# Performance work log

Measured on AMD Instinct MI355X. Metric: run time of the kernel, lower is better.

## Reference

```python
import jax, jax.numpy as jnp
import numpy as np

N_NODES = 50000
N_EDGES = 800000
IN_DIM = 128
HID = 64
HEADS = 4
SLOPE = 0.01


def edge_softmax(e, dst, n):
    # e: [E, H] logits, softmax over edges sharing the same destination node
    m = jax.ops.segment_max(e, dst, num_segments=n)          # [N, H]
    ex = jnp.exp(e - m[dst])                                 # [E, H]
    s = jax.ops.segment_sum(ex, dst, num_segments=n)         # [N, H]
    return ex / s[dst]


def gat_conv(h, src, dst, W, attn_l, attn_r, bias, n, heads, out_dim):
    ft = (h @ W).reshape(n, heads, out_dim)                  # [N, H, D]
    el = jnp.sum(ft * attn_l, axis=-1)                       # [N, H]
    er = jnp.sum(ft * attn_r, axis=-1)                       # [N, H]
    e = jax.nn.leaky_relu(el[src] + er[dst], SLOPE)          # [E, H]
    a = edge_softmax(e, dst, n)                              # [E, H]
    msg = ft[src] * a[:, :, None]                            # [E, H, D]
    out = jax.ops.segment_sum(msg, dst, num_segments=n)      # [N, H, D]
    return out + bias.reshape(1, heads, out_dim)


def setup_inputs() -> dict:
    key = jax.random.key(0)
    ks = jax.random.split(key, 12)
    inputs = jax.random.normal(ks[0], (N_NODES, IN_DIM), dtype=jnp.float32)
    src = jax.random.randint(ks[1], (N_EDGES,), 0, N_NODES, dtype=jnp.int32)
    dst = jax.random.randint(ks[2], (N_EDGES,), 0, N_NODES, dtype=jnp.int32)
    s1 = 1.0 / np.sqrt(IN_DIM)
    W1 = jax.random.normal(ks[3], (IN_DIM, HEADS * HID), dtype=jnp.float32) * s1
    al1 = jax.random.normal(ks[4], (HEADS, HID), dtype=jnp.float32) * 0.1
    ar1 = jax.random.normal(ks[5], (HEADS, HID), dtype=jnp.float32) * 0.1
    b1 = jnp.zeros((HEADS * HID,), dtype=jnp.float32)
    s2 = 1.0 / np.sqrt(HEADS * HID)
    W2 = jax.random.normal(ks[6], (HEADS * HID, HID), dtype=jnp.float32) * s2
    al2 = jax.random.normal(ks[7], (1, HID), dtype=jnp.float32) * 0.1
    ar2 = jax.random.normal(ks[8], (1, HID), dtype=jnp.float32) * 0.1
    b2 = jnp.zeros((HID,), dtype=jnp.float32)
    return {"inputs": inputs, "src": src, "dst": dst,
            "W1": W1, "al1": al1, "ar1": ar1, "b1": b1,
            "W2": W2, "al2": al2, "ar2": ar2, "b2": b2}


def reference(inputs, src, dst, W1, al1, ar1, b1, W2, al2, ar2, b2):
    # layer 1: multi-head, activation elu, flatten heads
    h = gat_conv(inputs, src, dst, W1, al1, ar1, b1, N_NODES, HEADS, HID)
    h = jax.nn.elu(h).reshape(N_NODES, HEADS * HID)
    # layer 2 (last): single head
    h = gat_conv(h, src, dst, W2, al2, ar2, b2, N_NODES, 1, HID)
    h = jax.nn.elu(h).reshape(N_NODES, HID)
    return h
```

## Files before the change

kernel.cpp:

```cpp
#include <hip/hip_runtime.h>
#include <hip/hip_bf16.h>
#include <math.h>

#define N_NODES 50000
#define N_EDGES 800000
#define IN_DIM 128
#define HID 64
#define HEADS 4

typedef unsigned short ushort_t;
typedef __attribute__((ext_vector_type(8))) short bf16x8;
typedef __attribute__((ext_vector_type(4))) float f32x4;

static __device__ __forceinline__ ushort_t f2bf(float f) {
  __hip_bfloat16 b = __float2bfloat16(f);
  return *(ushort_t*)&b;
}
static __device__ __forceinline__ float bflo(unsigned d) {
  union { unsigned u; float f; } c; c.u = d << 16; return c.f;
}
static __device__ __forceinline__ float bfhi(unsigned d) {
  union { unsigned u; float f; } c; c.u = d & 0xffff0000u; return c.f;
}
static __device__ __forceinline__ unsigned packbf(float lo, float hi) {
  return (unsigned)f2bf(lo) | ((unsigned)f2bf(hi) << 16);
}
static __device__ __forceinline__ float lrelu(float x) {
  return (x > 0.f) ? x : 0.01f * x;
}

__global__ __launch_bounds__(256) void k_cvt_hist(const float* __restrict__ w1,
                                                  const float* __restrict__ w2,
                                                  ushort_t* __restrict__ bpk1,
                                                  ushort_t* __restrict__ bpk2,
                                                  const int* __restrict__ dst,
                                                  int* __restrict__ cnt,
                                                  int* __restrict__ slot) {
  constexpr int NP1 = 4096;
  constexpr int NP2 = 2048;
  constexpr int CVT_BLK = (NP1 + NP2) / 256;
  int bid = blockIdx.x;
  if (bid < CVT_BLK) {
    int t = bid * 256 + threadIdx.x;
    if (t < NP1) {
      int l = t & 63, rem = t >> 6;
      int kk = rem & 3, ct = (rem >> 2) & 3, hh = rem >> 4;
      int kb = kk * 32 + (l >> 4) * 8;
      int col = hh * 64 + ct * 16 + (l & 15);
      ushort_t v[8];
      #pragma unroll
      for (int j = 0; j < 8; ++j) v[j] = f2bf(w1[(kb + j) * 256 + col]);
      *(uint4*)&bpk1[t * 8] = *(uint4*)v;
    } else {
      int u = t - NP1;
      int l = u & 63, rem = u >> 6;
      int kk = rem & 7, ct = rem >> 3;
      int kb = kk * 32 + (l >> 4) * 8;
      int col = ct * 16 + (l & 15);
      ushort_t v[8];
      #pragma unroll
      for (int j = 0; j < 8; ++j) v[j] = f2bf(w2[(kb + j) * 64 + col]);
      *(uint4*)&bpk2[u * 8] = *(uint4*)v;
    }
  } else {
    int e = (bid - CVT_BLK) * 256 + threadIdx.x;
    if (e < N_EDGES) {
      int d = dst[e];
      int p = atomicAdd(&cnt[d], 1);
      slot[e] = p;
    }
  }
}

__global__ __launch_bounds__(512) void k_scan_gemm1(const int* __restrict__ cnt,
                                                    int* __restrict__ offp,
                                                    int* __restrict__ bsum,
                                                    const float* __restrict__ A,
                                                    const ushort_t* __restrict__ Bpk,
                                                    ushort_t* __restrict__ C,
                                                    const float* __restrict__ al,
                                                    const float* __restrict__ ar,
                                                    float* __restrict__ el,
                                                    float* __restrict__ er, int M) {
  __shared__ char smraw[128 * 40 * 2];
  const int tid = threadIdx.x;
  if (blockIdx.x < 49) {
    int* lds = (int*)smraw;
    int i = blockIdx.x * 1024 + tid * 2;
    int v0 = (i < N_NODES) ? cnt[i] : 0;
    int v1 = (i + 1 < N_NODES) ? cnt[i + 1] : 0;
    int t = v0 + v1;
    lds[tid] = t;
    __syncthreads();
    for (int s = 1; s < 512; s <<= 1) {
      int u = (tid >= s) ? lds[tid - s] : 0;
      __syncthreads();
      lds[tid] += u;
      __syncthreads();
    }
    int excl = lds[tid] - t;
    if (i < N_NODES) offp[i] = excl;
    if (i + 1 < N_NODES) offp[i + 1] = excl + v0;
    if (tid == 511) bsum[blockIdx.x] = lds[511];
    return;
  }
  ushort_t (*As)[40] = (ushort_t(*)[40])smraw;
  const int m0 = (blockIdx.x - 49) * 128;
  const int w = tid >> 6, l = tid & 63;
  const int hh = w >> 1, rh = (w & 1) * 64;
  const int lr = l & 15, lk = l >> 4;
  f32x4 acc[4][4] = {};

  #pragma unroll
  for (int kk = 0; kk < 4; ++kk) {
    int k0 = kk * 32;
    {
      int r = tid >> 2, kc = (tid & 3) * 8;
      float4 va = make_float4(0.f, 0.f, 0.f, 0.f), vb = va;
      if (m0 + r < M) {
        va = *(const float4*)&A[(size_t)(m0 + r) * IN_DIM + k0 + kc];
        vb = *(const float4*)&A[(size_t)(m0 + r) * IN_DIM + k0 + kc + 4];
      }
      uint4 p;
      p.x = packbf(va.x, va.y); p.y = packbf(va.z, va.w);
      p.z = packbf(vb.x, vb.y); p.w = packbf(vb.z, vb.w);
      *(uint4*)&As[r][kc] = p;
    }
    __syncthreads();
    bf16x8 a[4];
    #pragma unroll
    for (int rt = 0; rt < 4; ++rt) a[rt] = *(const bf16x8*)&As[rh + rt * 16 + lr][lk * 8];
    #pragma unroll
    for (int ct = 0; ct < 4; ++ct) {
      bf16x8 b = ((const bf16x8*)Bpk)[((hh * 4 + ct) * 4 + kk) * 64 + l];
      #pragma unroll
      for (int rt = 0; rt < 4; ++rt)
        acc[rt][ct] = __builtin_amdgcn_mfma_f32_16x16x32_bf16(a[rt], b, acc[rt][ct], 0, 0, 0);
    }
    __syncthreads();
  }
  float ala[4], ara[4];
  #pragma unroll
  for (int ct = 0; ct < 4; ++ct) {
    ala[ct] = al[hh * 64 + ct * 16 + lr];
    ara[ct] = ar[hh * 64 + ct * 16 + lr];
  }
  #pragma unroll
  for (int rt = 0; rt < 4; ++rt)
    #pragma unroll
    for (int j = 0; j < 4; ++j) {
      float pel = 0.f, per = 0.f;
      #pragma unroll
      for (int ct = 0; ct < 4; ++ct) {
        float v = acc[rt][ct][j];
        pel = fmaf(v, ala[ct], pel);
        per = fmaf(v, ara[ct], per);
      }
      #pragma unroll
      for (int o = 1; o <= 8; o <<= 1) {
        pel += __shfl_xor(pel, o);
        per += __shfl_xor(per, o);
      }
      int row = m0 + rh + rt * 16 + lk * 4 + j;
      if (lr == 0 && row < M) { el[row * 4 + hh] = pel; er[row * 4 + hh] = per; }
    }
  #pragma unroll
  for (int rt = 0; rt < 4; ++rt)
    #pragma unroll
    for (int ct = 0; ct < 4; ++ct)
      #pragma unroll
      for (int j = 0; j < 4; ++j) {
        int row = m0 + rh + rt * 16 + lk * 4 + j;
        if (row < M) C[(size_t)row * 256 + hh * 64 + ct * 16 + lr] = f2bf(acc[rt][ct][j]);
      }
}

__global__ __launch_bounds__(256) void k_place(const int* __restrict__ offp,
                                               const int* __restrict__ bsum,
                                               int* __restrict__ off,
                                               const int* __restrict__ src,
                                               const int* __restrict__ dst,
                                               const int* __restrict__ slot,
                                               int* __restrict__ ssrc) {
  __shared__ int pref[64];
  const int tid = threadIdx.x;
  const int bid = blockIdx.x;
  if (bid < 49) {
    if (tid < 64) {
      int v = (tid < bid) ? bsum[tid] : 0;
      #pragma unroll
      for (int o = 1; o < 64; o <<= 1) v += __shfl_xor(v, o);
      if (tid == 0) pref[0] = v;
    }
    __syncthreads();
    int e0 = pref[0];
    int i = bid * 1024 + tid * 4;
    if (i + 3 < N_NODES) {
      int4 q = *(const int4*)&offp[i];
      *(int4*)&off[i] = make_int4(q.x + e0, q.y + e0, q.z + e0, q.w + e0);
    } else {
      if (i < N_NODES) off[i] = offp[i] + e0;
      if (i + 1 < N_NODES) off[i + 1] = offp[i + 1] + e0;
      if (i + 2 < N_NODES) off[i + 2] = offp[i + 2] + e0;
      if (i + 3 < N_NODES) off[i + 3] = offp[i + 3] + e0;
    }
    if (bid == 0 && tid == 0) off[N_NODES] = N_EDGES;
    return;
  }
  if (tid < 64) {
    int v = (tid < 49) ? bsum[tid] : 0;
    int orig = v;
    #pragma unroll
    for (int o = 1; o < 64; o <<= 1) { int u = __shfl_up(v, o); if (tid >= o) v += u; }
    pref[tid] = v - orig;
  }
  __syncthreads();
  int e = (bid - 49) * 256 + tid;
  if (e < N_EDGES) {
    int d = dst[e];
    ssrc[offp[d] + pref[d >> 10] + slot[e]] = src[e];
  }
}

__global__ __launch_bounds__(256) void agg4f_k(const ushort_t* __restrict__ ftb,
                                               const float* __restrict__ el,
                                               const float* __restrict__ er,
                                               const int* __restrict__ off,
                                               const int* __restrict__ ssrc,
                                               const float* __restrict__ bias,
                                               ushort_t* __restrict__ outb) {
  __shared__ float wl[4][64][4];
  __shared__ int srcl[4][64];
  int wv = threadIdx.x >> 6, lane = threadIdx.x & 63;
  int n = blockIdx.x * 4 + wv;
  if (n >= N_NODES) return;
  int s0 = off[n], s1 = off[n + 1];
  int half = lane >> 5, sl = lane & 31;
  int head = sl >> 3;
  const float4* el4 = (const float4*)el;
  float4 erv = ((const float4*)er)[n];
  float4 sum = make_float4(0.f, 0.f, 0.f, 0.f);
  float acc[8] = {};
  for (int c = s0; c < s1; c += 64) {
    int e = c + lane;
    float4 ex = make_float4(0.f, 0.f, 0.f, 0.f);
    int s = 0;
    if (e < s1) {
      s = ssrc[e];
      float4 q = el4[s];
      ex.x = __expf(lrelu(q.x + erv.x));
      ex.y = __expf(lrelu(q.y + erv.y));
      ex.z = __expf(lrelu(q.z + erv.z));
      ex.w = __expf(lrelu(q.w + erv.w));
      sum.x += ex.x; sum.y += ex.y; sum.z += ex.z; sum.w += ex.w;
    }
    srcl[wv][lane] = s;
    *(float4*)&wl[wv][lane][0] = ex;
    int cend = (c + 64 < s1) ? c + 64 : s1;
    #pragma unroll 4
    for (int i = c; i < cend; i += 2) {
      int e2 = i + half;
      if (e2 < cend) {
        int idx = e2 - c;
        int ss = srcl[wv][idx];
        float w = wl[wv][idx][head];
        uint4 u = *(const uint4*)&ftb[ss * 256 + sl * 8];
        acc[0] = fmaf(w, bflo(u.x), acc[0]);
        acc[1] = fmaf(w, bfhi(u.x), acc[1]);
        acc[2] = fmaf(w, bflo(u.y), acc[2]);
        acc[3] = fmaf(w, bfhi(u.y), acc[3]);
        acc[4] = fmaf(w, bflo(u.z), acc[4]);
        acc[5] = fmaf(w, bfhi(u.z), acc[5]);
        acc[6] = fmaf(w, bflo(u.w), acc[6]);
        acc[7] = fmaf(w, bfhi(u.w), acc[7]);
      }
    }
  }
  #pragma unroll
  for (int o = 1; o <= 32; o <<= 1) {
    sum.x += __shfl_xor(sum.x, o); sum.y += __shfl_xor(sum.y, o);
    sum.z += __shfl_xor(sum.z, o); sum.w += __shfl_xor(sum.w, o);
  }
  #pragma unroll
  for (int j = 0; j < 8; ++j) acc[j] += __shfl_xor(acc[j], 32);
  if (half == 0) {
    float sd = (head == 0) ? sum.x : (head == 1) ? sum.y : (head == 2) ? sum.z : sum.w;
    float rsv = (s1 > s0) ? 1.f / sd : 0.f;
    float4 b0 = ((const float4*)bias)[sl * 2];
    float4 b1 = ((const float4*)bias)[sl * 2 + 1];
    float o[8] = {fmaf(acc[0], rsv, b0.x), fmaf(acc[1], rsv, b0.y),
                  fmaf(acc[2], rsv, b0.z), fmaf(acc[3], rsv, b0.w),
                  fmaf(acc[4], rsv, b1.x), fmaf(acc[5], rsv, b1.y),
                  fmaf(acc[6], rsv, b1.z), fmaf(acc[7], rsv, b1.w)};
    #pragma unroll
    for (int j = 0; j < 8; ++j) o[j] = (o[j] > 0.f) ? o[j] : expm1f(o[j]);
    uint4 p;
    p.x = packbf(o[0], o[1]); p.y = packbf(o[2], o[3]);
    p.z = packbf(o[4], o[5]); p.w = packbf(o[6], o[7]);
    *(uint4*)&outb[n * 256 + sl * 8] = p;
  }
}

__global__ __launch_bounds__(512) void gemm2_mfma(const ushort_t* __restrict__ A,
                                                  const ushort_t* __restrict__ Bpk,
                                                  ushort_t* __restrict__ C,
                                                  const float* __restrict__ al,
                                                  const float* __restrict__ ar,
                                                  float* __restrict__ el,
                                                  float* __restrict__ er, int M) {
  __shared__ ushort_t As[128][40];
  const int tid = threadIdx.x;
  const int m0 = blockIdx.x * 128;
  const int w = tid >> 6, l = tid & 63;
  const int lr = l & 15, lk = l >> 4;
  f32x4 acc[4] = {};

  #pragma unroll
  for (int kk = 0; kk < 8; ++kk) {
    int k0 = kk * 32;
    {
      int r = tid >> 2, kc = (tid & 3) * 8;
      uint4 v = make_uint4(0, 0, 0, 0);
      if (m0 + r < M) v = *(const uint4*)&A[(size_t)(m0 + r) * 256 + k0 + kc];
      *(uint4*)&As[r][kc] = v;
    }
    __syncthreads();
    bf16x8 a = *(const bf16x8*)&As[w * 16 + lr][lk * 8];
    #pragma unroll
    for (int ct = 0; ct < 4; ++ct) {
      bf16x8 b = ((const bf16x8*)Bpk)[(ct * 8 + kk) * 64 + l];
      acc[ct] = __builtin_amdgcn_mfma_f32_16x16x32_bf16(a, b, acc[ct], 0, 0, 0);
    }
    __syncthreads();
  }
  float ala[4], ara[4];
  #pragma unroll
  for (int ct = 0; ct < 4; ++ct) {
    ala[ct] = al[ct * 16 + lr];
    ara[ct] = ar[ct * 16 + lr];
  }
  #pragma unroll
  for (int j = 0; j < 4; ++j) {
    float pel = 0.f, per = 0.f;
    #pragma unroll
    for (int ct = 0; ct < 4; ++ct) {
      float v = acc[ct][j];
      pel = fmaf(v, ala[ct], pel);
      per = fmaf(v, ara[ct], per);
    }
    #pragma unroll
    for (int o = 1; o <= 8; o <<= 1) {
      pel += __shfl_xor(pel, o);
      per += __shfl_xor(per, o);
    }
    int row = m0 + w * 16 + lk * 4 + j;
    if (lr == 0 && row < M) { el[row] = pel; er[row] = per; }
  }
  #pragma unroll
  for (int ct = 0; ct < 4; ++ct)
    #pragma unroll
    for (int j = 0; j < 4; ++j) {
      int row = m0 + w * 16 + lk * 4 + j;
      if (row < M) C[(size_t)row * 64 + ct * 16 + lr] = f2bf(acc[ct][j]);
    }
}

__global__ __launch_bounds__(256) void agg1f_k(const ushort_t* __restrict__ ftb,
                                               const float* __restrict__ el,
                                               const float* __restrict__ er,
                                               const int* __restrict__ off,
                                               const int* __restrict__ ssrc,
                                               const float* __restrict__ bias,
                                               float* __restrict__ out) {
  __shared__ float wl[4][64];
  __shared__ int srcl[4][64];
  int wv = threadIdx.x >> 6, lane = threadIdx.x & 63;
  int n = blockIdx.x * 4 + wv;
  if (n >= N_NODES) return;
  int s0 = off[n], s1 = off[n + 1];
  int g = lane >> 3, cg = lane & 7;
  float erv = er[n];
  float sum = 0.f;
  float acc[8] = {};
  for (int c = s0; c < s1; c += 64) {
    int e = c + lane;
    float ex = 0.f;
    int s = 0;
    if (e < s1) {
      s = ssrc[e];
      ex = __expf(lrelu(el[s] + erv));
      sum += ex;
    }
    srcl[wv][lane] = s;
    wl[wv][lane] = ex;
    int cend = (c + 64 < s1) ? c + 64 : s1;
    #pragma unroll 2
    for (int i = c; i < cend; i += 8) {
      int e2 = i + g;
      if (e2 < cend) {
        int idx = e2 - c;
        int ss = srcl[wv][idx];
        float w = wl[wv][idx];
        uint4 u = *(const uint4*)&ftb[ss * 64 + cg * 8];
        acc[0] = fmaf(w, bflo(u.x), acc[0]);
        acc[1] = fmaf(w, bfhi(u.x), acc[1]);
        acc[2] = fmaf(w, bflo(u.y), acc[2]);
        acc[3] = fmaf(w, bfhi(u.y), acc[3]);
        acc[4] = fmaf(w, bflo(u.z), acc[4]);
        acc[5] = fmaf(w, bfhi(u.z), acc[5]);
        acc[6] = fmaf(w, bflo(u.w), acc[6]);
        acc[7] = fmaf(w, bfhi(u.w), acc[7]);
      }
    }
  }
  #pragma unroll
  for (int o = 1; o <= 32; o <<= 1) sum += __shfl_xor(sum, o);
  #pragma unroll
  for (int o = 8; o <= 32; o <<= 1)
    #pragma unroll
    for (int j = 0; j < 8; ++j) acc[j] += __shfl_xor(acc[j], o);
  if (g == 0) {
    float rsv = (s1 > s0) ? 1.f / sum : 0.f;
    float4 b0 = ((const float4*)bias)[cg * 2];
    float4 b1 = ((const float4*)bias)[cg * 2 + 1];
    float o[8] = {fmaf(acc[0], rsv, b0.x), fmaf(acc[1], rsv, b0.y),
                  fmaf(acc[2], rsv, b0.z), fmaf(acc[3], rsv, b0.w),
                  fmaf(acc[4], rsv, b1.x), fmaf(acc[5], rsv, b1.y),
                  fmaf(acc[6], rsv, b1.z), fmaf(acc[7], rsv, b1.w)};
    #pragma unroll
    for (int j = 0; j < 8; ++j) o[j] = (o[j] > 0.f) ? o[j] : expm1f(o[j]);
    float4* out4 = (float4*)out;
    out4[(size_t)n * 16 + cg * 2]     = make_float4(o[0], o[1], o[2], o[3]);
    out4[(size_t)n * 16 + cg * 2 + 1] = make_float4(o[4], o[5], o[6], o[7]);
  }
}

extern "C" void kernel_launch(void* const* d_in, const int* in_sizes, int n_in,
                              void* d_out, int out_size, void* d_ws, size_t ws_size,
                              hipStream_t stream) {
  const float* x   = (const float*)d_in[0];
  const int*   src = (const int*)d_in[1];
  const int*   dst = (const int*)d_in[2];
  const float* W1  = (const float*)d_in[3];
  const float* al1 = (const float*)d_in[4];
  const float* ar1 = (const float*)d_in[5];
  const float* b1  = (const float*)d_in[6];
  const float* W2  = (const float*)d_in[7];
  const float* al2 = (const float*)d_in[8];
  const float* ar2 = (const float*)d_in[9];
  const float* b2  = (const float*)d_in[10];
  float* out = (float*)d_out;

  char* ws = (char*)d_ws;
  size_t wo = 0;
  auto alloc = [&](size_t b) { void* p = ws + wo; wo = (wo + b + 255) & ~(size_t)255; return p; };
  ushort_t* ft1b = (ushort_t*)alloc((size_t)N_NODES * 256 * 2);
  ushort_t* h1b  = (ushort_t*)alloc((size_t)N_NODES * 256 * 2);
  ushort_t* bpk1 = (ushort_t*)alloc((size_t)IN_DIM * 256 * 2);
  ushort_t* bpk2 = (ushort_t*)alloc((size_t)256 * 64 * 2);
  float* el1 = (float*)alloc((size_t)N_NODES * 4 * 4);
  float* er1 = (float*)alloc((size_t)N_NODES * 4 * 4);
  int*   off = (int*)alloc((size_t)(N_NODES + 1) * 4);
  int*   offp= (int*)alloc((size_t)N_NODES * 4);
  int*   cnt = (int*)alloc((size_t)N_NODES * 4);
  int*   slot= (int*)alloc((size_t)N_EDGES * 4);
  int*   bsum= (int*)alloc(256);
  int*   ssrc= (int*)alloc((size_t)N_EDGES * 4);
  ushort_t* ft2b = ft1b;
  float* el2 = el1, *er2 = er1;

  hipMemsetAsync(cnt, 0, (size_t)N_NODES * 4, stream);
  k_cvt_hist<<<24 + 3125, 256, 0, stream>>>(W1, W2, bpk1, bpk2, dst, cnt, slot);
  k_scan_gemm1<<<49 + 391, 512, 0, stream>>>(cnt, offp, bsum,
                                             x, bpk1, ft1b, al1, ar1, el1, er1, N_NODES);
  k_place<<<49 + 3125, 256, 0, stream>>>(offp, bsum, off, src, dst, slot, ssrc);
  agg4f_k<<<(N_NODES + 3) / 4, 256, 0, stream>>>(ft1b, el1, er1, off, ssrc, b1, h1b);
  gemm2_mfma<<<391, 512, 0, stream>>>(h1b, bpk2, ft2b, al2, ar2, el2, er2, N_NODES);
  agg1f_k<<<(N_NODES + 3) / 4, 256, 0, stream>>>(ft2b, el2, er2, off, ssrc, b2, out);
}
```

Baseline: 193.0 us.

## Fuse degree histogram into GEMM1 launch and split scan into its own kernel

Weight packing now gets its own small kernel. The edge-destination histogram (atomic counting) moves into the same launch as the layer-1 GEMM, so the two independent jobs share one grid. The prefix scan becomes a separate kernel after that, which adds one launch. The placement kernel now handles four edges per thread using int4 loads, which cuts its grid size, though the scattered writes stay scalar.

```diff
diff --git a/kernel.cpp b/kernel.cpp
--- a/kernel.cpp
+++ b/kernel.cpp
@@ -29,83 +29,53 @@
   return (x > 0.f) ? x : 0.01f * x;
 }
 
-__global__ __launch_bounds__(256) void k_cvt_hist(const float* __restrict__ w1,
-                                                  const float* __restrict__ w2,
-                                                  ushort_t* __restrict__ bpk1,
-                                                  ushort_t* __restrict__ bpk2,
-                                                  const int* __restrict__ dst,
-                                                  int* __restrict__ cnt,
-                                                  int* __restrict__ slot) {
-  constexpr int NP1 = 4096;
-  constexpr int NP2 = 2048;
-  constexpr int CVT_BLK = (NP1 + NP2) / 256;
-  int bid = blockIdx.x;
-  if (bid < CVT_BLK) {
-    int t = bid * 256 + threadIdx.x;
-    if (t < NP1) {
-      int l = t & 63, rem = t >> 6;
-      int kk = rem & 3, ct = (rem >> 2) & 3, hh = rem >> 4;
-      int kb = kk * 32 + (l >> 4) * 8;
-      int col = hh * 64 + ct * 16 + (l & 15);
-      ushort_t v[8];
-      #pragma unroll
-      for (int j = 0; j < 8; ++j) v[j] = f2bf(w1[(kb + j) * 256 + col]);
-      *(uint4*)&bpk1[t * 8] = *(uint4*)v;
-    } else {
-      int u = t - NP1;
-      int l = u & 63, rem = u >> 6;
-      int kk = rem & 7, ct = rem >> 3;
-      int kb = kk * 32 + (l >> 4) * 8;
-      int col = ct * 16 + (l & 15);
-      ushort_t v[8];
-      #pragma unroll
-      for (int j = 0; j < 8; ++j) v[j] = f2bf(w2[(kb + j) * 64 + col]);
-      *(uint4*)&bpk2[u * 8] = *(uint4*)v;
-    }
-  } else {
-    int e = (bid - CVT_BLK) * 256 + threadIdx.x;
+__global__ __launch_bounds__(512) void k0_pack(const float* __restrict__ w1,
+                                               const float* __restrict__ w2,
+                                               ushort_t* __restrict__ bpk1,
+                                               ushort_t* __restrict__ bpk2) {
+  int t = blockIdx.x * 512 + threadIdx.x;
+  if (t < 4096) {
+    int l = t & 63, rem = t >> 6;
+    int kk = rem & 3, ct = (rem >> 2) & 3, hh = rem >> 4;
+    int kb = kk * 32 + (l >> 4) * 8;
+    int col = hh * 64 + ct * 16 + (l & 15);
+    ushort_t v[8];
+    #pragma unroll
+    for (int j = 0; j < 8; ++j) v[j] = f2bf(w1[(kb + j) * 256 + col]);
+    *(uint4*)&bpk1[t * 8] = *(uint4*)v;
+  } else if (t < 6144) {
+    int u = t - 4096;
+    int l = u & 63, rem = u >> 6;
+    int kk = rem & 7, ct = rem >> 3;
+    int kb = kk * 32 + (l >> 4) * 8;
+    int col = ct * 16 + (l & 15);
+    ushort_t v[8];
+    #pragma unroll
+    for (int j = 0; j < 8; ++j) v[j] = f2bf(w2[(kb + j) * 64 + col]);
+    *(uint4*)&bpk2[u * 8] = *(uint4*)v;
+  }
+}
+
+__global__ __launch_bounds__(512) void k_gemm1_hist(
+    const float* __restrict__ A, const ushort_t* __restrict__ Bpk,
+    ushort_t* __restrict__ C, const float* __restrict__ al,
+    const float* __restrict__ ar, float* __restrict__ el,
+    float* __restrict__ er,
+    const int* __restrict__ dst, int* __restrict__ cnt,
+    int* __restrict__ slot) {
+  __shared__ ushort_t As[128][40];
+  const int tid = threadIdx.x;
+  const int bid = blockIdx.x;
+  if (bid >= 391) {
+    int e = (bid - 391) * 512 + tid;
     if (e < N_EDGES) {
       int d = dst[e];
       int p = atomicAdd(&cnt[d], 1);
       slot[e] = p;
     }
-  }
-}
-
-__global__ __launch_bounds__(512) void k_scan_gemm1(const int* __restrict__ cnt,
-                                                    int* __restrict__ offp,
-                                                    int* __restrict__ bsum,
-                                                    const float* __restrict__ A,
-                                                    const ushort_t* __restrict__ Bpk,
-                                                    ushort_t* __restrict__ C,
-                                                    const float* __restrict__ al,
-                                                    const float* __restrict__ ar,
-                                                    float* __restrict__ el,
-                                                    float* __restrict__ er, int M) {
-  __shared__ char smraw[128 * 40 * 2];
-  const int tid = threadIdx.x;
-  if (blockIdx.x < 49) {
-    int* lds = (int*)smraw;
-    int i = blockIdx.x * 1024 + tid * 2;
-    int v0 = (i < N_NODES) ? cnt[i] : 0;
-    int v1 = (i + 1 < N_NODES) ? cnt[i + 1] : 0;
-    int t = v0 + v1;
-    lds[tid] = t;
-    __syncthreads();
-    for (int s = 1; s < 512; s <<= 1) {
-      int u = (tid >= s) ? lds[tid - s] : 0;
-      __syncthreads();
-      lds[tid] += u;
-      __syncthreads();
-    }
-    int excl = lds[tid] - t;
-    if (i < N_NODES) offp[i] = excl;
-    if (i + 1 < N_NODES) offp[i + 1] = excl + v0;
-    if (tid == 511) bsum[blockIdx.x] = lds[511];
     return;
   }
-  ushort_t (*As)[40] = (ushort_t(*)[40])smraw;
-  const int m0 = (blockIdx.x - 49) * 128;
+  const int m0 = bid * 128;
   const int w = tid >> 6, l = tid & 63;
   const int hh = w >> 1, rh = (w & 1) * 64;
   const int lr = l & 15, lk = l >> 4;
@@ -117,7 +87,7 @@
     {
       int r = tid >> 2, kc = (tid & 3) * 8;
       float4 va = make_float4(0.f, 0.f, 0.f, 0.f), vb = va;
-      if (m0 + r < M) {
+      if (m0 + r < N_NODES) {
         va = *(const float4*)&A[(size_t)(m0 + r) * IN_DIM + k0 + kc];
         vb = *(const float4*)&A[(size_t)(m0 + r) * IN_DIM + k0 + kc + 4];
       }
@@ -162,7 +132,7 @@
         per += __shfl_xor(per, o);
       }
       int row = m0 + rh + rt * 16 + lk * 4 + j;
-      if (lr == 0 && row < M) { el[row * 4 + hh] = pel; er[row * 4 + hh] = per; }
+      if (lr == 0 && row < N_NODES) { el[row * 4 + hh] = pel; er[row * 4 + hh] = per; }
     }
   #pragma unroll
   for (int rt = 0; rt < 4; ++rt)
@@ -171,8 +141,31 @@
       #pragma unroll
       for (int j = 0; j < 4; ++j) {
         int row = m0 + rh + rt * 16 + lk * 4 + j;
-        if (row < M) C[(size_t)row * 256 + hh * 64 + ct * 16 + lr] = f2bf(acc[rt][ct][j]);
-      }
+        if (row < N_NODES) C[(size_t)row * 256 + hh * 64 + ct * 16 + lr] = f2bf(acc[rt][ct][j]);
+      }
+}
+
+__global__ __launch_bounds__(512) void k_scan(const int* __restrict__ cnt,
+                                              int* __restrict__ offp,
+                                              int* __restrict__ bsum) {
+  __shared__ int lds[512];
+  const int tid = threadIdx.x;
+  int i = blockIdx.x * 1024 + tid * 2;
+  int v0 = (i < N_NODES) ? cnt[i] : 0;
+  int v1 = (i + 1 < N_NODES) ? cnt[i + 1] : 0;
+  int t = v0 + v1;
+  lds[tid] = t;
+  __syncthreads();
+  for (int s = 1; s < 512; s <<= 1) {
+    int u = (tid >= s) ? lds[tid - s] : 0;
+    __syncthreads();
+    lds[tid] += u;
+    __syncthreads();
+  }
+  int excl = lds[tid] - t;
+  if (i < N_NODES) offp[i] = excl;
+  if (i + 1 < N_NODES) offp[i + 1] = excl + v0;
+  if (tid == 511) bsum[blockIdx.x] = lds[511];
 }
 
 __global__ __launch_bounds__(256) void k_place(const int* __restrict__ offp,
@@ -215,10 +208,15 @@
     pref[tid] = v - orig;
   }
   __syncthreads();
-  int e = (bid - 49) * 256 + tid;
-  if (e < N_EDGES) {
-    int d = dst[e];
-    ssrc[offp[d] + pref[d >> 10] + slot[e]] = src[e];
+  int e0 = (bid - 49) * 1024 + tid * 4;
+  if (e0 < N_EDGES) {
+    int4 d4 = *(const int4*)&dst[e0];
+    int4 s4 = *(const int4*)&src[e0];
+    int4 p4 = *(const int4*)&slot[e0];
+    ssrc[offp[d4.x] + pref[d4.x >> 10] + p4.x] = s4.x;
+    ssrc[offp[d4.y] + pref[d4.y >> 10] + p4.y] = s4.y;
+    ssrc[offp[d4.z] + pref[d4.z >> 10] + p4.z] = s4.z;
+    ssrc[offp[d4.w] + pref[d4.w >> 10] + p4.w] = s4.w;
   }
 }
 
@@ -470,10 +468,11 @@
   float* el2 = el1, *er2 = er1;
 
   hipMemsetAsync(cnt, 0, (size_t)N_NODES * 4, stream);
-  k_cvt_hist<<<24 + 3125, 256, 0, stream>>>(W1, W2, bpk1, bpk2, dst, cnt, slot);
-  k_scan_gemm1<<<49 + 391, 512, 0, stream>>>(cnt, offp, bsum,
-                                             x, bpk1, ft1b, al1, ar1, el1, er1, N_NODES);
-  k_place<<<49 + 3125, 256, 0, stream>>>(offp, bsum, off, src, dst, slot, ssrc);
+  k0_pack<<<12, 512, 0, stream>>>(W1, W2, bpk1, bpk2);
+  k_gemm1_hist<<<391 + 1563, 512, 0, stream>>>(
+      x, bpk1, ft1b, al1, ar1, el1, er1, dst, cnt, slot);
+  k_scan<<<49, 512, 0, stream>>>(cnt, offp, bsum);
+  k_place<<<49 + 782, 256, 0, stream>>>(offp, bsum, off, src, dst, slot, ssrc);
   agg4f_k<<<(N_NODES + 3) / 4, 256, 0, stream>>>(ft1b, el1, er1, off, ssrc, b1, h1b);
   gemm2_mfma<<<391, 512, 0, stream>>>(h1b, bpk2, ft2b, al2, ar2, el2, er2, N_NODES);
   agg1f_k<<<(N_NODES + 3) / 4, 256, 0, stream>>>(ft2b, el2, er2, off, ssrc, b2, out);
```

Measured after the change: 188.1 us. 1.03x faster.
